# Kernel tuning notes

Hardware: AMD Instinct MI355X
Metric: run time of the kernel (lower is better)

The kernel has to match this reference:

```python
import jax, jax.numpy as jnp
import numpy as np

B, T_ENC, U = 8, 200, 100
VOCAB, ENC_DIM, PRED_DIM, EMBED_DIM = 1024, 512, 512, 128


def setup_inputs() -> dict:
    key = jax.random.key(0)
    ks = jax.random.split(key, 13)
    n = lambda k, shape, fan_in: (jax.random.normal(k, shape, jnp.float32) / np.sqrt(fan_in)).astype(jnp.float32)
    return {
        "enc_out": jax.random.normal(ks[0], (B, T_ENC, ENC_DIM), jnp.float32),
        "targets": jax.random.randint(ks[1], (B, U), 0, VOCAB, jnp.int32),
        "target_len": jnp.full((B,), U, jnp.int32),
        # params
        "emb_table": n(ks[2], (VOCAB + 1, EMBED_DIM), 1.0),
        "W_ih": n(ks[3], (4 * PRED_DIM, EMBED_DIM), EMBED_DIM),
        "W_hh": n(ks[4], (4 * PRED_DIM, PRED_DIM), PRED_DIM),
        "b_ih": jnp.zeros((4 * PRED_DIM,), jnp.float32),
        "b_hh": jnp.zeros((4 * PRED_DIM,), jnp.float32),
        "W_enc": n(ks[5], (PRED_DIM, ENC_DIM), ENC_DIM),
        "b_enc": jnp.zeros((PRED_DIM,), jnp.float32),
        "W_pred": n(ks[6], (PRED_DIM, PRED_DIM), PRED_DIM),
        "b_pred": jnp.zeros((PRED_DIM,), jnp.float32),
        "W_joint": n(ks[7], (VOCAB + 1, PRED_DIM), PRED_DIM),
        "b_joint": jnp.zeros((VOCAB + 1,), jnp.float32),
    }


def reference(enc_out, targets, target_len, emb_table, W_ih, W_hh, b_ih, b_hh,
              W_enc, b_enc, W_pred, b_pred, W_joint, b_joint):
    # targets_with_blank: prepend blank_id = vocab_size
    blank_id = emb_table.shape[0] - 1
    Bsz = targets.shape[0]
    tw = jnp.concatenate([jnp.full((Bsz, 1), blank_id, targets.dtype), targets], axis=1)
    emb = emb_table[tw]  # (B, U+1, E)

    P = W_hh.shape[1]
    h0 = jnp.zeros((Bsz, P), emb.dtype)

    def lstm_step(carry, x_t):
        h, c = carry
        gates = x_t @ W_ih.T + b_ih + h @ W_hh.T + b_hh  # (B, 4P)
        i, f, g, o = jnp.split(gates, 4, axis=-1)  # PyTorch LSTMCell gate order
        i, f, o = jax.nn.sigmoid(i), jax.nn.sigmoid(f), jax.nn.sigmoid(o)
        c = f * c + i * jnp.tanh(g)
        h = o * jnp.tanh(c)
        return (h, c), h

    _, pred = jax.lax.scan(lstm_step, (h0, h0), jnp.swapaxes(emb, 0, 1))
    pred = jnp.swapaxes(pred, 0, 1)  # (B, U+1, P)

    f_enc = enc_out @ W_enc.T + b_enc   # (B, T, P)
    f_pred = pred @ W_pred.T + b_pred   # (B, U+1, P)
    joint = jnp.tanh(f_enc[:, :, None, :] + f_pred[:, None, :, :])  # (B, T, U+1, P)
    logits = joint @ W_joint.T + b_joint  # (B, T, U+1, V+1)
    return logits
```

## Files before the change

kernel.cpp:

```cpp
#include <hip/hip_runtime.h>
#include <stdint.h>
#include <stddef.h>

#define BB 8
#define TENC 200
#define UU 100
#define UP1 101
#define VP1 1025
#define ED 128
#define PD 512
#define LSTM_NWG 64
#define MTOT 161600
#define MB_  20200

typedef __attribute__((ext_vector_type(8))) unsigned short ushort8;
typedef __attribute__((ext_vector_type(8))) __bf16 bf16x8;
typedef __attribute__((ext_vector_type(4))) float f32x4;

__device__ __forceinline__ float bf2f(unsigned short u){
  unsigned int x = ((unsigned int)u) << 16;
  return __builtin_bit_cast(float, x);
}
__device__ __forceinline__ unsigned short f2bf(float f){
  unsigned int x = __builtin_bit_cast(unsigned int, f);
  unsigned int r = (x + 0x7fffu + ((x >> 16) & 1u)) >> 16;
  return (unsigned short)r;
}
__device__ __forceinline__ float tanh_fast(float x){
  float e = __expf(2.0f * x);
  return 1.0f - 2.0f / (e + 1.0f);
}
__device__ __forceinline__ float sigm(float x){
  return 1.0f / (1.0f + __expf(-x));
}
__device__ __forceinline__ void gload_lds16(const unsigned short* gsrc, unsigned short* ldst){
  __builtin_amdgcn_global_load_lds((const __attribute__((address_space(1))) void*)gsrc,
                                   (__attribute__((address_space(3))) void*)ldst, 16, 0, 0);
}

__global__ __launch_bounds__(256) void k_cvt_bf16(const float* __restrict__ src,
                                                  unsigned short* __restrict__ dst, int n){
  int i = blockIdx.x * 256 + threadIdx.x;
  if (i < n) dst[i] = f2bf(src[i]);
}

__global__ __launch_bounds__(256) void k_xgate(
    const float* __restrict__ emb, const int* __restrict__ targets,
    const float* __restrict__ W_ih, const float* __restrict__ b_ih,
    const float* __restrict__ b_hh, float* __restrict__ xg)
{
  __shared__ float e_s[BB * ED];
  const int u  = blockIdx.x >> 2;
  const int jq = blockIdx.x & 3;
  const int tid = threadIdx.x;
  for (int idx = tid; idx < BB * ED; idx += 256){
    int b = idx >> 7, e = idx & 127;
    int tok = (u == 0) ? 1024 : targets[b * UU + (u - 1)];
    e_s[idx] = emb[(size_t)tok * ED + e];
  }
  __syncthreads();
  float acc[2][BB];
  #pragma unroll
  for (int r = 0; r < 2; r++)
    #pragma unroll
    for (int b = 0; b < BB; b++) acc[r][b] = 0.0f;
  const int j0 = jq * 512 + tid;
  const float* w0p = W_ih + (size_t)j0 * ED;
  const float* w1p = W_ih + (size_t)(j0 + 256) * ED;
  for (int e = 0; e < ED; e++){
    float w0 = w0p[e], w1 = w1p[e];
    #pragma unroll
    for (int b = 0; b < BB; b++){
      float ev = e_s[b * ED + e];
      acc[0][b] = fmaf(ev, w0, acc[0][b]);
      acc[1][b] = fmaf(ev, w1, acc[1][b]);
    }
  }
  #pragma unroll
  for (int r = 0; r < 2; r++){
    int j = j0 + r * 256;
    float bias = b_ih[j] + b_hh[j];
    #pragma unroll
    for (int b = 0; b < BB; b++)
      xg[((size_t)b * UP1 + u) * 2048 + j] = acc[r][b] + bias;
  }
}

__global__ __launch_bounds__(256) void k_lstm_all(
    const float* __restrict__ xg, const float* __restrict__ W_hh,
    float* __restrict__ pred, float* __restrict__ hb, unsigned int* __restrict__ seq)
{
  __shared__ float h_s[8][520];
  __shared__ float red[32 * 257];
  __shared__ float gates_s[32][9];
  const int tid = threadIdx.x;
  const int wg  = blockIdx.x;
  const int p0  = wg * 8;
  const int jg = tid >> 5, kc = tid & 31;
  const float* wrow[4];
  #pragma unroll
  for (int r = 0; r < 4; r++){
    int jl = jg * 4 + r;
    int grow = (jl >> 3) * PD + p0 + (jl & 7);
    wrow[r] = W_hh + (size_t)grow * PD;
  }
  float c_reg = 0.0f;
  for (int u = 0; u < UP1; u++){
    float xi = 0.f, xf = 0.f, xgv = 0.f, xo = 0.f;
    if (tid < 64){
      int pl = tid >> 3, b = tid & 7;
      const float* xr = xg + ((size_t)(b * UP1 + u)) * 2048;
      int p = p0 + pl;
      xi = xr[p]; xf = xr[512 + p]; xgv = xr[1024 + p]; xo = xr[1536 + p];
    }
    if (u > 0){
      if (tid < 64){
        while (1){
          unsigned int v = __hip_atomic_load(&seq[tid * 16], __ATOMIC_RELAXED, __HIP_MEMORY_SCOPE_AGENT);
          if (__all(v >= (unsigned int)u)) break;
          __builtin_amdgcn_s_sleep(1);
        }
      }
      __syncthreads();
      const float* hsrc = hb + ((u - 1) & 1) * 4096;
      float tmp[16];
      #pragma unroll
      for (int j = 0; j < 16; j++)
        tmp[j] = __hip_atomic_load(hsrc + tid + 256 * j,
                                   __ATOMIC_RELAXED, __HIP_MEMORY_SCOPE_AGENT);
      #pragma unroll
      for (int j = 0; j < 16; j++){
        int i = tid + 256 * j;
        h_s[i >> 9][i & 511] = tmp[j];
      }
    } else {
      for (int i = tid; i < 8 * PD; i += 256) h_s[i >> 9][i & 511] = 0.0f;
    }
    __syncthreads();
    float acc[4][BB];
    #pragma unroll
    for (int r = 0; r < 4; r++)
      #pragma unroll
      for (int b = 0; b < BB; b++) acc[r][b] = 0.0f;
    for (int i = 0; i < 16; i++){
      int k = kc + 32 * i;
      float hv[BB];
      #pragma unroll
      for (int b = 0; b < BB; b++) hv[b] = h_s[b][k];
      #pragma unroll
      for (int r = 0; r < 4; r++){
        float wv = wrow[r][k];
        #pragma unroll
        for (int b = 0; b < BB; b++) acc[r][b] = fmaf(hv[b], wv, acc[r][b]);
      }
    }
    #pragma unroll
    for (int r = 0; r < 4; r++)
      #pragma unroll
      for (int b = 0; b < BB; b++)
        red[kc * 257 + jg * 32 + r * 8 + b] = acc[r][b];
    __syncthreads();
    {
      int jl = tid >> 3, b = tid & 7;
      float s = 0.0f;
      #pragma unroll
      for (int kk = 0; kk < 32; kk++)
        s += red[kk * 257 + (jl >> 2) * 32 + (jl & 3) * 8 + b];
      gates_s[jl][b] = s;
    }
    __syncthreads();
    if (tid < 64){
      int pl = tid >> 3, b2 = tid & 7;
      int p = p0 + pl;
      float gi = gates_s[0  + pl][b2] + xi;
      float gf = gates_s[8  + pl][b2] + xf;
      float gg = gates_s[16 + pl][b2] + xgv;
      float go = gates_s[24 + pl][b2] + xo;
      float iv = sigm(gi), fv = sigm(gf), ov = sigm(go);
      c_reg = fv * c_reg + iv * tanh_fast(gg);
      float hval = ov * tanh_fast(c_reg);
      __hip_atomic_store(hb + (u & 1) * 4096 + b2 * 512 + p, hval,
                         __ATOMIC_RELAXED, __HIP_MEMORY_SCOPE_AGENT);
      pred[((size_t)(b2 * UP1 + u)) * PD + p] = hval;
    }
    if (u < UP1 - 1 && tid == 0){
      asm volatile("s_waitcnt vmcnt(0)" ::: "memory");
      __hip_atomic_store(&seq[wg * 16], (unsigned int)(u + 1),
                         __ATOMIC_RELAXED, __HIP_MEMORY_SCOPE_AGENT);
    }
  }
}

__global__ __launch_bounds__(256) void k_gemm_bias_bf16(
    const float* __restrict__ A, const float* __restrict__ W,
    const float* __restrict__ bias, unsigned short* __restrict__ out, int M)
{
  __shared__ float a_s[16][68];
  __shared__ float b_s[16][68];
  const int m0 = blockIdx.x * 64, n0 = blockIdx.y * 64;
  const int tid = threadIdx.x;
  const int tx = tid & 15, ty = tid >> 4;
  float acc[4][4];
  #pragma unroll
  for (int i2 = 0; i2 < 4; i2++)
    #pragma unroll
    for (int j2 = 0; j2 < 4; j2++) acc[i2][j2] = 0.0f;
  for (int k0 = 0; k0 < 512; k0 += 16){
    int mm = tid >> 2, k4 = (tid & 3) * 4;
    int row = m0 + mm; if (row >= M) row = M - 1;
    float4 av = *(const float4*)(A + (size_t)row * 512 + k0 + k4);
    a_s[k4 + 0][mm] = av.x; a_s[k4 + 1][mm] = av.y;
    a_s[k4 + 2][mm] = av.z; a_s[k4 + 3][mm] = av.w;
    float4 bv = *(const float4*)(W + (size_t)(n0 + mm) * 512 + k0 + k4);
    b_s[k4 + 0][mm] = bv.x; b_s[k4 + 1][mm] = bv.y;
    b_s[k4 + 2][mm] = bv.z; b_s[k4 + 3][mm] = bv.w;
    __syncthreads();
    #pragma unroll
    for (int k = 0; k < 16; k++){
      float4 a4 = *(const float4*)&a_s[k][ty * 4];
      float4 b4 = *(const float4*)&b_s[k][tx * 4];
      float aa[4] = {a4.x, a4.y, a4.z, a4.w};
      float bb[4] = {b4.x, b4.y, b4.z, b4.w};
      #pragma unroll
      for (int i2 = 0; i2 < 4; i2++)
        #pragma unroll
        for (int j2 = 0; j2 < 4; j2++)
          acc[i2][j2] = fmaf(aa[i2], bb[j2], acc[i2][j2]);
    }
    __syncthreads();
  }
  #pragma unroll
  for (int i2 = 0; i2 < 4; i2++){
    int m = m0 + ty * 4 + i2;
    if (m < M){
      #pragma unroll
      for (int j2 = 0; j2 < 4; j2++){
        int n = n0 + tx * 4 + j2;
        out[(size_t)m * 512 + n] = f2bf(acc[i2][j2] + bias[n]);
      }
    }
  }
}

__global__ __launch_bounds__(256) void k_tanhA(
    const unsigned short* __restrict__ fe, const unsigned short* __restrict__ fp,
    const unsigned short* __restrict__ wj, const float* __restrict__ bj,
    unsigned short* __restrict__ Aout, float* __restrict__ out,
    int m_base, int M_cnt)
{
  const int tid = threadIdx.x;
  const int mlocal = blockIdx.x * 4 + (tid >> 6);
  if (mlocal >= M_cnt) return;
  const int l = tid & 63;
  const int m = m_base + mlocal;
  const int q = m / 101;
  const int u = m - q * 101;
  const int b = q / 200;
  ushort8 f8 = *(const ushort8*)(fe + (size_t)q * 512 + l * 8);
  ushort8 p8 = *(const ushort8*)(fp + (size_t)(b * 101 + u) * 512 + l * 8);
  ushort8 w8 = *(const ushort8*)(wj + (size_t)1024 * 512 + l * 8);
  ushort8 a;
  float s = 0.0f;
  #pragma unroll
  for (int e = 0; e < 8; e++){
    float v = tanh_fast(bf2f(f8[e]) + bf2f(p8[e]));
    a[e] = f2bf(v);
    s += v * bf2f(w8[e]);
  }
  *(ushort8*)(Aout + (size_t)mlocal * 512 + l * 8) = a;
  #pragma unroll
  for (int off = 1; off < 64; off <<= 1) s += __shfl_xor(s, off);
  if (l == 0) out[(size_t)m * VP1 + 1024] = s + bj[1024];
}

__global__ __launch_bounds__(256, 4) void k_joint7s(
    const unsigned short* __restrict__ A, const unsigned short* __restrict__ wj,
    const float* __restrict__ bj, float* __restrict__ out,
    int m_base, int M_cnt, int nmt)
{
  __shared__ unsigned short A_s[2][128 * 32];
  __shared__ unsigned short B_s[2][128 * 32];
  const int bid = blockIdx.x;
  const int mt  = (bid >> 6) * 8 + (bid & 7);
  if (mt >= nmt) return;
  const int m0 = mt * 128;
  const int n0 = ((bid >> 3) & 7) * 128;
  const int tid = threadIdx.x;
  const int w = tid >> 6, l = tid & 63;
  const int l15 = l & 15, lg = l >> 4;
  const int wr = w >> 1, wc = w & 1;

  auto stage = [&](int buf, int kc){
    #pragma unroll
    for (int i = 0; i < 2; i++){
      int sbase = i * 256 + w * 64;
      int slot  = sbase + l;
      int r  = slot >> 2;
      int cs = slot & 3;
      int col8 = cs ^ ((r >> 1) & 3);
      int ra = m0 + r; if (ra >= M_cnt) ra = M_cnt - 1;
      gload_lds16(A + (size_t)ra * 512 + kc * 32 + col8 * 8,
                  (unsigned short*)A_s[buf] + (size_t)sbase * 8);
      gload_lds16(wj + (size_t)(n0 + r) * 512 + kc * 32 + col8 * 8,
                  (unsigned short*)B_s[buf] + (size_t)sbase * 8);
    }
  };

  stage(0, 0);
  __syncthreads();

  f32x4 acc[4][4];
  #pragma unroll
  for (int fr = 0; fr < 4; fr++)
    #pragma unroll
    for (int fc = 0; fc < 4; fc++)
      acc[fr][fc] = (f32x4){0.f, 0.f, 0.f, 0.f};

  for (int kc = 0; kc < 16; kc++){
    const int buf = kc & 1;
    if (kc < 15){
      stage(buf ^ 1, kc + 1);
      asm volatile("s_waitcnt vmcnt(4)" ::: "memory");
    } else {
      asm volatile("s_waitcnt vmcnt(0)" ::: "memory");
    }
    __builtin_amdgcn_s_barrier();

    bf16x8 afr[4], bfr[4];
    #pragma unroll
    for (int f = 0; f < 4; f++){
      int ra = wr * 64 + f * 16 + l15;
      int bya = ra * 64 + ((lg ^ ((ra >> 1) & 3)) * 16);
      afr[f] = __builtin_bit_cast(bf16x8, *(const ushort8*)((const char*)A_s[buf] + bya));
      int rb = wc * 64 + f * 16 + l15;
      int byb = rb * 64 + ((lg ^ ((rb >> 1) & 3)) * 16);
      bfr[f] = __builtin_bit_cast(bf16x8, *(const ushort8*)((const char*)B_s[buf] + byb));
    }
    #pragma unroll
    for (int fr = 0; fr < 4; fr++)
      #pragma unroll
      for (int fc = 0; fc < 4; fc++)
        acc[fr][fc] = __builtin_amdgcn_mfma_f32_16x16x32_bf16(bfr[fc], afr[fr], acc[fr][fc], 0, 0, 0);
    __builtin_amdgcn_s_barrier();
  }

  #pragma unroll
  for (int fr = 0; fr < 4; fr++){
    int mloc = m0 + wr * 64 + fr * 16 + l15;
    if (mloc < M_cnt){
      float* orow = out + (size_t)(m_base + mloc) * VP1;
      #pragma unroll
      for (int fc = 0; fc < 4; fc++){
        int col = n0 + wc * 64 + fc * 16 + lg * 4;
        float4 bv = *(const float4*)(bj + col);
        f32x4 v = acc[fr][fc];
        float4 st = {v[0] + bv.x, v[1] + bv.y, v[2] + bv.z, v[3] + bv.w};
        *(float4*)(orow + col) = st;
      }
    }
  }
}

extern "C" void kernel_launch(void* const* d_in, const int* in_sizes, int n_in,
                              void* d_out, int out_size, void* d_ws, size_t ws_size,
                              hipStream_t stream) {
  const float* enc_out = (const float*)d_in[0];
  const int*   targets = (const int*)d_in[1];
  const float* emb     = (const float*)d_in[3];
  const float* W_ih    = (const float*)d_in[4];
  const float* W_hh    = (const float*)d_in[5];
  const float* b_ih    = (const float*)d_in[6];
  const float* b_hh    = (const float*)d_in[7];
  const float* W_enc   = (const float*)d_in[8];
  const float* b_enc   = (const float*)d_in[9];
  const float* W_pred  = (const float*)d_in[10];
  const float* b_pred  = (const float*)d_in[11];
  const float* W_joint = (const float*)d_in[12];
  const float* b_joint = (const float*)d_in[13];
  float* out = (float*)d_out;

  char* ws = (char*)d_ws;
  float* xg            = (float*)(ws + 0);
  float* pred          = (float*)(ws + 6619136);
  unsigned short* feb  = (unsigned short*)(ws + 8273920);
  unsigned short* fpb  = (unsigned short*)(ws + 9912320);
  unsigned short* wjb  = (unsigned short*)(ws + 10739712);
  float* hb            = (float*)(ws + 11789312);
  unsigned int* seq    = (unsigned int*)(ws + 11822080);
  unsigned short* Abuf = (unsigned short*)(ws + 11827200);
  const size_t FULL_NEED  = 11827200 + (size_t)MTOT * 512 * 2;
  const size_t BATCH_NEED = 11827200 + (size_t)MB_  * 512 * 2;

  (void)hipMemsetAsync(seq, 0, 4096, stream);
  hipLaunchKernelGGL(k_cvt_bf16, dim3((VP1 * 512 + 255) / 256), dim3(256), 0, stream,
                     W_joint, wjb, VP1 * 512);
  hipLaunchKernelGGL(k_xgate, dim3(404), dim3(256), 0, stream,
                     emb, targets, W_ih, b_ih, b_hh, xg);
  hipLaunchKernelGGL(k_gemm_bias_bf16, dim3(25, 8), dim3(256), 0, stream,
                     enc_out, W_enc, b_enc, feb, 1600);
  hipLaunchKernelGGL(k_lstm_all, dim3(LSTM_NWG), dim3(256), 0, stream,
                     xg, W_hh, pred, hb, seq);
  hipLaunchKernelGGL(k_gemm_bias_bf16, dim3(13, 8), dim3(256), 0, stream,
                     pred, W_pred, b_pred, fpb, 808);

  if (ws_size >= FULL_NEED){
    const int nmt = 1263;
    const int grid = 8 * 8 * ((nmt + 7) / 8);
    hipLaunchKernelGGL(k_tanhA, dim3(MTOT / 4), dim3(256), 0, stream,
                       feb, fpb, wjb, b_joint, Abuf, out, 0, MTOT);
    hipLaunchKernelGGL(k_joint7s, dim3(grid), dim3(256), 0, stream,
                       Abuf, wjb, b_joint, out, 0, MTOT, nmt);
  } else if (ws_size >= BATCH_NEED){
    const int nmt = 158;
    const int grid = 8 * 8 * ((nmt + 7) / 8);
    for (int b = 0; b < 8; b++){
      hipLaunchKernelGGL(k_tanhA, dim3(MB_ / 4), dim3(256), 0, stream,
                         feb, fpb, wjb, b_joint, Abuf, out, b * MB_, MB_);
      hipLaunchKernelGGL(k_joint7s, dim3(grid), dim3(256), 0, stream,
                         Abuf, wjb, b_joint, out, b * MB_, MB_, nmt);
    }
  } else {
    const int nmt = 40;
    const int grid = 8 * 8 * ((nmt + 7) / 8);
    for (int c = 0; c < 32; c++){
      hipLaunchKernelGGL(k_tanhA, dim3(5050 / 2, 1), dim3(256), 0, stream,
                         feb, fpb, wjb, b_joint, Abuf, out, c * 5050, 5050);
      hipLaunchKernelGGL(k_joint7s, dim3(grid), dim3(256), 0, stream,
                         Abuf, wjb, b_joint, out, c * 5050, 5050, nmt);
    }
  }
}
```

Baseline: 860.3 us.

## Overlap encoder projection GEMM with LSTM recurrence in one launch; fold seq memset

Merges the encoder projection GEMM into the persistent LSTM kernel as 200 extra workgroups, so the projection runs on otherwise idle CUs while the 64 LSTM workgroups step through the recurrence. It also drops the separate hipMemsetAsync of the sequence counters by zeroing them in the first block of the bf16 conversion kernel. The aim is to hide the encoder GEMM and one launch behind the latency-bound LSTM. The risk is that the LSTM uses spin-wait synchronisation across workgroups, so it depends on all 64 LSTM blocks being co-resident; the extra blocks and the larger shared union could delay scheduling or steal bandwidth.

After: 835.9 us. 2.8% less time.

```diff
diff --git a/kernel.cpp b/kernel.cpp
--- a/kernel.cpp
+++ b/kernel.cpp
@@ -39,7 +39,12 @@
 }
 
 __global__ __launch_bounds__(256) void k_cvt_bf16(const float* __restrict__ src,
-                                                  unsigned short* __restrict__ dst, int n){
+                                                  unsigned short* __restrict__ dst, int n,
+                                                  unsigned int* __restrict__ seq){
+  if (blockIdx.x == 0){
+    #pragma unroll
+    for (int j = 0; j < 4; j++) seq[threadIdx.x + 256 * j] = 0u;
+  }
   int i = blockIdx.x * 256 + threadIdx.x;
   if (i < n) dst[i] = f2bf(src[i]);
 }
@@ -86,14 +91,67 @@
   }
 }
 
-__global__ __launch_bounds__(256) void k_lstm_all(
+__global__ __launch_bounds__(256) void k_lstm_enc(
     const float* __restrict__ xg, const float* __restrict__ W_hh,
-    float* __restrict__ pred, float* __restrict__ hb, unsigned int* __restrict__ seq)
+    float* __restrict__ pred, float* __restrict__ hb, unsigned int* __restrict__ seq,
+    const float* __restrict__ encA, const float* __restrict__ W_enc,
+    const float* __restrict__ b_enc, unsigned short* __restrict__ feb)
 {
-  __shared__ float h_s[8][520];
-  __shared__ float red[32 * 257];
-  __shared__ float gates_s[32][9];
+  __shared__ char smem[50688];
   const int tid = threadIdx.x;
+
+  if (blockIdx.x >= LSTM_NWG){
+    float (*a_s)[68] = (float(*)[68])smem;
+    float (*b_s)[68] = (float(*)[68])(smem + 4352);
+    const int bid2 = blockIdx.x - LSTM_NWG;
+    const int m0 = (bid2 % 25) * 64, n0 = (bid2 / 25) * 64;
+    const int tx = tid & 15, ty = tid >> 4;
+    float acc[4][4];
+    #pragma unroll
+    for (int i2 = 0; i2 < 4; i2++)
+      #pragma unroll
+      for (int j2 = 0; j2 < 4; j2++) acc[i2][j2] = 0.0f;
+    for (int k0 = 0; k0 < 512; k0 += 16){
+      int mm = tid >> 2, k4 = (tid & 3) * 4;
+      int row = m0 + mm; if (row >= 1600) row = 1599;
+      float4 av = *(const float4*)(encA + (size_t)row * 512 + k0 + k4);
+      a_s[k4 + 0][mm] = av.x; a_s[k4 + 1][mm] = av.y;
+      a_s[k4 + 2][mm] = av.z; a_s[k4 + 3][mm] = av.w;
+      float4 bv = *(const float4*)(W_enc + (size_t)(n0 + mm) * 512 + k0 + k4);
+      b_s[k4 + 0][mm] = bv.x; b_s[k4 + 1][mm] = bv.y;
+      b_s[k4 + 2][mm] = bv.z; b_s[k4 + 3][mm] = bv.w;
+      __syncthreads();
+      #pragma unroll
+      for (int k = 0; k < 16; k++){
+        float4 a4 = *(const float4*)&a_s[k][ty * 4];
+        float4 b4 = *(const float4*)&b_s[k][tx * 4];
+        float aa[4] = {a4.x, a4.y, a4.z, a4.w};
+        float bb[4] = {b4.x, b4.y, b4.z, b4.w};
+        #pragma unroll
+        for (int i2 = 0; i2 < 4; i2++)
+          #pragma unroll
+          for (int j2 = 0; j2 < 4; j2++)
+            acc[i2][j2] = fmaf(aa[i2], bb[j2], acc[i2][j2]);
+      }
+      __syncthreads();
+    }
+    #pragma unroll
+    for (int i2 = 0; i2 < 4; i2++){
+      int m = m0 + ty * 4 + i2;
+      if (m < 1600){
+        #pragma unroll
+        for (int j2 = 0; j2 < 4; j2++){
+          int n = n0 + tx * 4 + j2;
+          feb[(size_t)m * 512 + n] = f2bf(acc[i2][j2] + b_enc[n]);
+        }
+      }
+    }
+    return;
+  }
+
+  float (*h_s)[520]    = (float(*)[520])smem;
+  float *red           = (float*)(smem + 16640);
+  float (*gates_s)[9]  = (float(*)[9])(smem + 16640 + 32896);
   const int wg  = blockIdx.x;
   const int p0  = wg * 8;
   const int jg = tid >> 5, kc = tid & 31;
@@ -391,15 +449,12 @@
   const size_t FULL_NEED  = 11827200 + (size_t)MTOT * 512 * 2;
   const size_t BATCH_NEED = 11827200 + (size_t)MB_  * 512 * 2;
 
-  (void)hipMemsetAsync(seq, 0, 4096, stream);
   hipLaunchKernelGGL(k_cvt_bf16, dim3((VP1 * 512 + 255) / 256), dim3(256), 0, stream,
-                     W_joint, wjb, VP1 * 512);
+                     W_joint, wjb, VP1 * 512, seq);
   hipLaunchKernelGGL(k_xgate, dim3(404), dim3(256), 0, stream,
                      emb, targets, W_ih, b_ih, b_hh, xg);
-  hipLaunchKernelGGL(k_gemm_bias_bf16, dim3(25, 8), dim3(256), 0, stream,
-                     enc_out, W_enc, b_enc, feb, 1600);
-  hipLaunchKernelGGL(k_lstm_all, dim3(LSTM_NWG), dim3(256), 0, stream,
-                     xg, W_hh, pred, hb, seq);
+  hipLaunchKernelGGL(k_lstm_enc, dim3(LSTM_NWG + 200), dim3(256), 0, stream,
+                     xg, W_hh, pred, hb, seq, enc_out, W_enc, b_enc, feb);
   hipLaunchKernelGGL(k_gemm_bias_bf16, dim3(13, 8), dim3(256), 0, stream,
                      pred, W_pred, b_pred, fpb, 808);
 
```
